# Kernel optimization log

Hardware: AMD Instinct MI355X
Metric: run time of the kernel (lower is better)

The kernel has to match this reference:

```python
import jax, jax.numpy as jnp
import numpy as np

NBITS = 3      # weight LSQ bits
PBITS = 8      # partial-sum LSQ bits
EPS = 1e-5


def round_ste(x):
    # straight-through round: identity gradient
    return x + jax.lax.stop_gradient(jnp.round(x) - x)


def lsq(x, alpha, nbits):
    # learned-step-size quantize/dequantize (symmetric signed)
    qn = -(2 ** (nbits - 1))
    qp = 2 ** (nbits - 1) - 1
    return round_ste(jnp.clip(x / alpha, qn, qp)) * alpha


def split_views(x):
    # x: [B,C,H,W] -> 9 shifted views of the 1-padded input, stacked [9,B,C,H,W]
    B, C, H, W = x.shape
    xp = jnp.pad(x, ((0, 0), (0, 0), (1, 1), (1, 1)))
    views = [xp[:, :, di:di + H, dj:dj + W] for dj in range(3) for di in range(3)]
    return jnp.stack(views, 0)


def split_conv3x3(x, w, wa, pa):
    # 3x3 conv emulated as 9 shifted 1x1 LSQ convs with quantized partial-sum accumulate
    # w: [9,O,C] per-tap 1x1 weights, wa: [9] weight step sizes, pa: [9] psum step sizes
    xs = split_views(x)                                      # [9,B,C,H,W]
    wq = jax.vmap(lambda wk, ak: lsq(wk, ak, NBITS))(w, wa)  # [9,O,C]
    ps = jnp.einsum('kbchw,koc->kbohw', xs, wq)              # 9 partial sums
    psq = lsq(ps, pa[:, None, None, None, None], PBITS)      # PartialSumLSQ each tap
    return psq.sum(0)                                        # accumulate -> [B,O,H,W]


def batchnorm(x, g, b):
    m = x.mean((0, 2, 3), keepdims=True)
    v = x.var((0, 2, 3), keepdims=True)
    return (x - m) / jnp.sqrt(v + EPS) * g[None, :, None, None] + b[None, :, None, None]


def setup_inputs() -> dict:
    key = jax.random.key(0)
    ks = jax.random.split(key, 8)
    B, C, O, H, W = 16, 128, 128, 56, 56
    x = jax.random.normal(ks[0], (B, C, H, W), jnp.float32)
    w1 = jax.random.normal(ks[1], (9, O, C), jnp.float32) * 0.05
    w2 = jax.random.normal(ks[2], (9, O, O), jnp.float32) * 0.05
    qp_w = 2 ** (NBITS - 1) - 1
    wa1 = 2.0 * jnp.mean(jnp.abs(w1), axis=(1, 2)) / np.sqrt(qp_w)
    wa2 = 2.0 * jnp.mean(jnp.abs(w2), axis=(1, 2)) / np.sqrt(qp_w)
    pa1 = jnp.full((9,), 0.05, jnp.float32)
    pa2 = jnp.full((9,), 0.05, jnp.float32)
    g1 = jnp.ones((O,), jnp.float32); b1 = jnp.zeros((O,), jnp.float32)
    g2 = jnp.ones((O,), jnp.float32); b2 = jnp.zeros((O,), jnp.float32)
    return {'x': x, 'w1': w1, 'wa1': wa1, 'pa1': pa1, 'g1': g1, 'b1': b1,
            'w2': w2, 'wa2': wa2, 'pa2': pa2, 'g2': g2, 'b2': b2}


def reference(x, w1, wa1, pa1, g1, b1, w2, wa2, pa2, g2, b2):
    identity = x
    out = split_conv3x3(x, w1, wa1, pa1)
    out = jax.nn.relu(batchnorm(out, g1, b1))
    out = split_conv3x3(out, w2, wa2, pa2)
    out = batchnorm(out, g2, b2)
    return jax.nn.relu(out + identity)
```

## Files before the change

### kernel.cpp

```cpp
#include <hip/hip_runtime.h>
#include <math.h>

typedef _Float16 f16;
typedef _Float16 half8 __attribute__((ext_vector_type(8)));
typedef float floatx16 __attribute__((ext_vector_type(16)));
typedef unsigned int u32;

#define HW_     3136
#define NPC     50176.0f
#define PB      3364
#define PPLANE  53824
#define ASTRIDE (2 * PPLANE * 16)

#define SW(c, px) (((px) + ((c) >> 2) + ((c) & 3) * 8) & 63)

typedef __attribute__((address_space(3))) u32 lds_u32;
typedef __attribute__((address_space(1))) u32 glb_u32;
__device__ __forceinline__ void async_copy16(const void* g, void* l) {
    __builtin_amdgcn_global_load_lds((const glb_u32*)g, (lds_u32*)l, 16, 0, 0);
}

__global__ __launch_bounds__(256) void setup_kernel(
        const float* __restrict__ w1, const float* __restrict__ wa1,
        const float* __restrict__ w2, const float* __restrict__ wa2,
        f16* __restrict__ W2a, f16* __restrict__ W2b, char* __restrict__ X2) {
    const int idx = blockIdx.x * 256 + threadIdx.x;
    if (idx < 36864) {
        const float* w;
        const float* wa;
        f16* o;
        int m;
        if (idx < 18432) { w = w1; wa = wa1; o = W2a; m = idx; }
        else             { w = w2; wa = wa2; o = W2b; m = idx - 18432; }
        const int tap = m >> 11;
        const int r = m & 2047;
        const int k2 = r >> 7;
        const int oc = r & 127;
        const float a = wa[tap];
        const float* src = w + ((size_t)(tap * 128 + oc) * 128 + k2 * 8);
        half8 hv;
#pragma unroll
        for (int j = 0; j < 8; ++j)
            hv[j] = (f16)rintf(fminf(fmaxf(src[j] / a, -4.f), 3.f));
        *(half8*)(o + (size_t)m * 8) = hv;
    } else {
        const int m = idx - 36864;
        const int k2 = m / 3648;
        const int r = m - k2 * 3648;
        const int b = r / 228;
        const int j = r - b * 228;
        int h, w;
        if (j < 58)        { h = 0;  w = j; }
        else if (j < 116)  { h = 57; w = j - 58; }
        else { const int k = j - 116; h = 1 + (k >> 1); w = (k & 1) * 57; }
        const size_t chunk = (size_t)k2 * PPLANE + (size_t)b * PB + h * 58 + w;
        float4 z = {0.f, 0.f, 0.f, 0.f};
        *(float4*)(X2 + chunk * 16) = z;
    }
}

__global__ __launch_bounds__(256) void pack_kernel(
        const float* __restrict__ x, char* __restrict__ X2,
        float* __restrict__ stats) {
    const int t = threadIdx.x;
    const int blk = blockIdx.x;
    if (blk == 0 && t < 512) stats[t] = 0.f;
    const int b = blk / 49;
    const int p0 = (blk - b * 49) * 64;
    const int px = t & 63;
    const int cq = t >> 6;
    const int p = p0 + px;
    const int h = p / 56;
    const int w = p - h * 56;
    const size_t pp = (size_t)b * PB + (h + 1) * 58 + (w + 1);
    const float* xb = x + (size_t)b * 128 * HW_ + p;
#pragma unroll
    for (int s = 0; s < 4; ++s) {
        const int cg = s * 4 + cq;
        half8 hv, lv;
#pragma unroll
        for (int j = 0; j < 8; ++j) {
            const float v = xb[(size_t)(cg * 8 + j) * HW_];
            const f16 hh = (f16)v;
            hv[j] = hh;
            lv[j] = (f16)(v - (float)hh);
        }
        *(half8*)(X2 + ((size_t)cg * PPLANE + pp) * 16) = hv;
        *(half8*)(X2 + ((size_t)(cg + 16) * PPLANE + pp) * 16) = lv;
    }
}

__global__ __launch_bounds__(256, 2) void conv_kernel(
        const char* __restrict__ X2, const char* __restrict__ W2,
        const float* __restrict__ wav, const float* __restrict__ pav,
        float* __restrict__ cbuf, float* __restrict__ stats) {
    __shared__ f16 Bls[2][16384];
    __shared__ float red[512];
    const int t = threadIdx.x;
    const int lane = t & 63;
    const int wv = t >> 6;
    const int wm = wv & 1, wn = wv >> 1;
    const int tile = (blockIdx.x & 7) * 98 + (blockIdx.x >> 3);
    const int kh = lane >> 5;
    const int ln = lane & 31;

    const int gp = tile * 64 + wm * 32 + ln;
    const int b = gp / HW_;
    const int p = gp - b * HW_;
    const int h = p / 56;
    const int w = p - h * 56;
    const int ppad = b * PB + (h + 1) * 58 + (w + 1);

    const int bdsoff0 = (kh * 128 + wn * 64 + ln) * 16;
    const int bdsoff1 = bdsoff0 + 32 * 16;
    const int sbase = wv * 8;

    floatx16 facc[2];
#pragma unroll
    for (int nt = 0; nt < 2; ++nt)
#pragma unroll
        for (int r = 0; r < 16; ++r) facc[nt][r] = 0.f;

#pragma unroll
    for (int i = 0; i < 8; ++i)
        async_copy16(W2 + (((sbase + i) * 64 + lane) << 4),
                     (void*)&Bls[0][(sbase + i) * 512]);
    const int aoff0 = ((ppad - 59) + kh * PPLANE) << 4;
    half8 afr[16];
#pragma unroll
    for (int c = 0; c < 16; ++c)
        afr[c] = *(const half8*)(X2 + aoff0 + c * ASTRIDE);
    __syncthreads();

    for (int tap = 0; tap < 9; ++tap) {
        const float pak = pav[tap];
        const float s1 = wav[tap] / pak;
        const char* bcur = (const char*)&Bls[tap & 1][0];
        int aoffn = 0;
        if (tap < 8) {
            const char* wt = W2 + (tap + 1) * 32768;
            f16* bnxt = &Bls[(tap + 1) & 1][0];
#pragma unroll
            for (int i = 0; i < 8; ++i)
                async_copy16(wt + (((sbase + i) * 64 + lane) << 4),
                             (void*)&bnxt[(sbase + i) * 512]);
            const int dn = ((tap + 1) % 3 - 1) * 58 + ((tap + 1) / 3 - 1);
            aoffn = ((ppad + dn) + kh * PPLANE) << 4;
        }
        half8 bds[2][8];
#pragma unroll
        for (int kf = 0; kf < 8; ++kf) {
            bds[0][kf] = *(const half8*)(bcur + kf * 4096 + bdsoff0);
            bds[1][kf] = *(const half8*)(bcur + kf * 4096 + bdsoff1);
        }

        floatx16 acc[2];
#pragma unroll
        for (int nt = 0; nt < 2; ++nt)
#pragma unroll
            for (int r = 0; r < 16; ++r) acc[nt][r] = 0.f;

#pragma unroll
        for (int s = 0; s < 16; ++s) {
            acc[0] = __builtin_amdgcn_mfma_f32_32x32x16_f16(
                afr[s], bds[0][s & 7], acc[0], 0, 0, 0);
            acc[1] = __builtin_amdgcn_mfma_f32_32x32x16_f16(
                afr[s], bds[1][s & 7], acc[1], 0, 0, 0);
            if (tap < 8)
                afr[s] = *(const half8*)(X2 + aoffn + s * ASTRIDE);
        }

#pragma unroll
        for (int nt = 0; nt < 2; ++nt)
#pragma unroll
            for (int r = 0; r < 16; ++r) {
                const float q = rintf(
                    __builtin_amdgcn_fmed3f(acc[nt][r] * s1, -128.f, 127.f));
                facc[nt][r] = fmaf(q, pak, facc[nt][r]);
            }
        __syncthreads();
    }

    const int gpb = tile * 64 + wm * 32;
#pragma unroll
    for (int r = 0; r < 16; ++r) {
        const int row = (r & 3) + 8 * (r >> 2) + 4 * kh;
        float* rp = cbuf + (size_t)(gpb + row) * 128 + wn * 64 + ln;
        rp[0]  = facc[0][r];
        rp[32] = facc[1][r];
    }

    float sv[2], qv[2];
#pragma unroll
    for (int nt = 0; nt < 2; ++nt) {
        float s = 0.f, q = 0.f;
#pragma unroll
        for (int r = 0; r < 16; ++r) {
            const float v = facc[nt][r];
            s += v;
            q = fmaf(v, v, q);
        }
        s += __shfl_xor(s, 32, 64);
        q += __shfl_xor(q, 32, 64);
        sv[nt] = s; qv[nt] = q;
    }
    if (lane < 32) {
#pragma unroll
        for (int nt = 0; nt < 2; ++nt) {
            const int oc = wn * 64 + nt * 32 + lane;
            red[oc * 2 + wm] = sv[nt];
            red[256 + oc * 2 + wm] = qv[nt];
        }
    }
    __syncthreads();
    if (t < 128) {
        atomicAdd(&stats[t],       red[2 * t] + red[2 * t + 1]);
        atomicAdd(&stats[128 + t], red[256 + 2 * t] + red[256 + 2 * t + 1]);
    }
}

__global__ __launch_bounds__(256) void bn_split_kernel(
        const float* __restrict__ cbuf, const float* __restrict__ stats,
        const float* __restrict__ g, const float* __restrict__ bb,
        char* __restrict__ X2) {
    __shared__ float xs[8192];
    __shared__ float scs[128], shs[128];
    const int t = threadIdx.x;
    if (t < 128) {
        const float m = stats[t] * (1.f / NPC);
        const float var = stats[128 + t] * (1.f / NPC) - m * m;
        const float inv = 1.f / sqrtf(var + 1e-5f);
        const float sc = g[t] * inv;
        scs[t] = sc;
        shs[t] = bb[t] - m * sc;
    }
    __syncthreads();
    const int blk = blockIdx.x;
#pragma unroll
    for (int i = 0; i < 8; ++i) {
        const int idx = i * 256 + t;
        const int px = idx >> 5;
        const int q = idx & 31;
        const float4 v = *(const float4*)&cbuf[(size_t)(blk * 64 + px) * 128 + q * 4];
        const float vv[4] = {v.x, v.y, v.z, v.w};
#pragma unroll
        for (int j = 0; j < 4; ++j) {
            const int c = q * 4 + j;
            xs[c * 64 + SW(c, px)] = fmaxf(fmaf(vv[j], scs[c], shs[c]), 0.f);
        }
    }
    __syncthreads();
    const int b = blk / 49;
    const int p0 = (blk - b * 49) * 64;
    const int px = t & 63;
    const int cq = t >> 6;
    const int p = p0 + px;
    const int h = p / 56;
    const int w = p - h * 56;
    const size_t pp = (size_t)b * PB + (h + 1) * 58 + (w + 1);
#pragma unroll
    for (int s = 0; s < 4; ++s) {
        const int cg = s * 4 + cq;
        half8 hv, lv;
#pragma unroll
        for (int j = 0; j < 8; ++j) {
            const int c = cg * 8 + j;
            const float v = xs[c * 64 + SW(c, px)];
            const f16 hh = (f16)v;
            hv[j] = hh;
            lv[j] = (f16)(v - (float)hh);
        }
        *(half8*)(X2 + ((size_t)cg * PPLANE + pp) * 16) = hv;
        *(half8*)(X2 + ((size_t)(cg + 16) * PPLANE + pp) * 16) = lv;
    }
}

__global__ __launch_bounds__(256) void final_kernel(
        const float* __restrict__ cbuf, const float* __restrict__ stats,
        const float* __restrict__ g, const float* __restrict__ bb,
        const float* __restrict__ resid, float* __restrict__ out) {
    __shared__ float xs[8192];
    __shared__ float scs[128], shs[128];
    const int t = threadIdx.x;
    if (t < 128) {
        const float m = stats[t] * (1.f / NPC);
        const float var = stats[128 + t] * (1.f / NPC) - m * m;
        const float inv = 1.f / sqrtf(var + 1e-5f);
        const float sc = g[t] * inv;
        scs[t] = sc;
        shs[t] = bb[t] - m * sc;
    }
    __syncthreads();
    const int blk = blockIdx.x;
#pragma unroll
    for (int i = 0; i < 8; ++i) {
        const int idx = i * 256 + t;
        const int px = idx >> 5;
        const int q = idx & 31;
        const float4 v = *(const float4*)&cbuf[(size_t)(blk * 64 + px) * 128 + q * 4];
        const float vv[4] = {v.x, v.y, v.z, v.w};
#pragma unroll
        for (int j = 0; j < 4; ++j) {
            const int c = q * 4 + j;
            xs[c * 64 + SW(c, px)] = fmaf(vv[j], scs[c], shs[c]);
        }
    }
    __syncthreads();
    const int b = blk / 49;
    const int p0 = (blk - b * 49) * 64;
    const int lane = t & 63, wq = t >> 6;
#pragma unroll
    for (int i = 0; i < 32; ++i) {
        const int c = i * 4 + wq;
        const float v = xs[c * 64 + SW(c, lane)];
        const size_t gi = (size_t)(b * 128 + c) * HW_ + p0 + lane;
        out[gi] = fmaxf(v + resid[gi], 0.f);
    }
}

extern "C" void kernel_launch(void* const* d_in, const int* in_sizes, int n_in,
                              void* d_out, int out_size, void* d_ws, size_t ws_size,
                              hipStream_t stream) {
    const float* x   = (const float*)d_in[0];
    const float* w1  = (const float*)d_in[1];
    const float* wa1 = (const float*)d_in[2];
    const float* pa1 = (const float*)d_in[3];
    const float* g1  = (const float*)d_in[4];
    const float* b1  = (const float*)d_in[5];
    const float* w2  = (const float*)d_in[6];
    const float* wa2 = (const float*)d_in[7];
    const float* pa2 = (const float*)d_in[8];
    const float* g2  = (const float*)d_in[9];
    const float* b2  = (const float*)d_in[10];
    float* out = (float*)d_out;

    char* ws = (char*)d_ws;
    char*  X2    = ws;
    float* cbuf  = (float*)(ws + 27557888);
    f16*   W2a   = (f16*)(ws + 53248000);
    f16*   W2b   = (f16*)(ws + 53542912);
    float* stats = (float*)(ws + 53837824);
    float* stats1 = stats;
    float* stats2 = stats + 256;

    hipLaunchKernelGGL(setup_kernel, dim3(600), dim3(256), 0, stream,
                       w1, wa1, w2, wa2, W2a, W2b, X2);
    hipLaunchKernelGGL(pack_kernel, dim3(784), dim3(256), 0, stream,
                       x, X2, stats);
    hipLaunchKernelGGL(conv_kernel, dim3(784), dim3(256), 0, stream,
                       X2, (const char*)W2a, wa1, pa1, cbuf, stats1);
    hipLaunchKernelGGL(bn_split_kernel, dim3(784), dim3(256), 0, stream,
                       cbuf, stats1, g1, b1, X2);
    hipLaunchKernelGGL(conv_kernel, dim3(784), dim3(256), 0, stream,
                       X2, (const char*)W2b, wa2, pa2, cbuf, stats2);
    hipLaunchKernelGGL(final_kernel, dim3(784), dim3(256), 0, stream,
                       cbuf, stats2, g2, b2, x, out);
}
```

Measured before the change: 230.7 us.

## Retile conv to 128px x 64oc blocks and merge setup with pack

Each conv block now covers 128 pixels with 4 waves stacked along M and only half of the output channels. That halves the per-tap weight tile in LDS and asks for 4 blocks per CU instead of 2. The stats reduction is rewritten to sum over 4 waves per channel half. Separately, the weight-quantize/border-zero setup kernel and the input pack kernel are merged into one launch to save a kernel boundary. The trade-off is that the activation fragments are now read by two blocks each, and the higher occupancy target may force register spills given the large per-thread fragment arrays.

```diff
diff --git a/kernel.cpp b/kernel.cpp
--- a/kernel.cpp
+++ b/kernel.cpp
@@ -20,12 +20,41 @@
     __builtin_amdgcn_global_load_lds((const glb_u32*)g, (lds_u32*)l, 16, 0, 0);
 }
 
-__global__ __launch_bounds__(256) void setup_kernel(
+__global__ __launch_bounds__(256) void prelude_kernel(
+        const float* __restrict__ x, char* __restrict__ X2,
         const float* __restrict__ w1, const float* __restrict__ wa1,
         const float* __restrict__ w2, const float* __restrict__ wa2,
-        f16* __restrict__ W2a, f16* __restrict__ W2b, char* __restrict__ X2) {
-    const int idx = blockIdx.x * 256 + threadIdx.x;
-    if (idx < 36864) {
+        f16* __restrict__ W2a, f16* __restrict__ W2b,
+        float* __restrict__ stats) {
+    const int t = threadIdx.x;
+    if (blockIdx.x < 784) {
+        const int blk = blockIdx.x;
+        if (blk == 0 && t < 512) stats[t] = 0.f;
+        const int b = blk / 49;
+        const int p0 = (blk - b * 49) * 64;
+        const int px = t & 63;
+        const int cq = t >> 6;
+        const int p = p0 + px;
+        const int h = p / 56;
+        const int w = p - h * 56;
+        const size_t pp = (size_t)b * PB + (h + 1) * 58 + (w + 1);
+        const float* xb = x + (size_t)b * 128 * HW_ + p;
+#pragma unroll
+        for (int s = 0; s < 4; ++s) {
+            const int cg = s * 4 + cq;
+            half8 hv, lv;
+#pragma unroll
+            for (int j = 0; j < 8; ++j) {
+                const float v = xb[(size_t)(cg * 8 + j) * HW_];
+                const f16 hh = (f16)v;
+                hv[j] = hh;
+                lv[j] = (f16)(v - (float)hh);
+            }
+            *(half8*)(X2 + ((size_t)cg * PPLANE + pp) * 16) = hv;
+            *(half8*)(X2 + ((size_t)(cg + 16) * PPLANE + pp) * 16) = lv;
+        }
+    } else if (blockIdx.x < 928) {
+        const int idx = (blockIdx.x - 784) * 256 + t;
         const float* w;
         const float* wa;
         f16* o;
@@ -44,7 +73,7 @@
             hv[j] = (f16)rintf(fminf(fmaxf(src[j] / a, -4.f), 3.f));
         *(half8*)(o + (size_t)m * 8) = hv;
     } else {
-        const int m = idx - 36864;
+        const int m = (blockIdx.x - 928) * 256 + t;
         const int k2 = m / 3648;
         const int r = m - k2 * 3648;
         const int b = r / 228;
@@ -59,61 +88,32 @@
     }
 }
 
-__global__ __launch_bounds__(256) void pack_kernel(
-        const float* __restrict__ x, char* __restrict__ X2,
-        float* __restrict__ stats) {
-    const int t = threadIdx.x;
-    const int blk = blockIdx.x;
-    if (blk == 0 && t < 512) stats[t] = 0.f;
-    const int b = blk / 49;
-    const int p0 = (blk - b * 49) * 64;
-    const int px = t & 63;
-    const int cq = t >> 6;
-    const int p = p0 + px;
-    const int h = p / 56;
-    const int w = p - h * 56;
-    const size_t pp = (size_t)b * PB + (h + 1) * 58 + (w + 1);
-    const float* xb = x + (size_t)b * 128 * HW_ + p;
-#pragma unroll
-    for (int s = 0; s < 4; ++s) {
-        const int cg = s * 4 + cq;
-        half8 hv, lv;
-#pragma unroll
-        for (int j = 0; j < 8; ++j) {
-            const float v = xb[(size_t)(cg * 8 + j) * HW_];
-            const f16 hh = (f16)v;
-            hv[j] = hh;
-            lv[j] = (f16)(v - (float)hh);
-        }
-        *(half8*)(X2 + ((size_t)cg * PPLANE + pp) * 16) = hv;
-        *(half8*)(X2 + ((size_t)(cg + 16) * PPLANE + pp) * 16) = lv;
-    }
-}
-
-__global__ __launch_bounds__(256, 2) void conv_kernel(
+__global__ __launch_bounds__(256, 4) void conv_kernel(
         const char* __restrict__ X2, const char* __restrict__ W2,
         const float* __restrict__ wav, const float* __restrict__ pav,
         float* __restrict__ cbuf, float* __restrict__ stats) {
-    __shared__ f16 Bls[2][16384];
+    __shared__ f16 Bls[2][8192];
     __shared__ float red[512];
     const int t = threadIdx.x;
     const int lane = t & 63;
     const int wv = t >> 6;
-    const int wm = wv & 1, wn = wv >> 1;
-    const int tile = (blockIdx.x & 7) * 98 + (blockIdx.x >> 3);
+    const int blk = (blockIdx.x & 7) * 98 + (blockIdx.x >> 3);
+    const int tile = blk >> 1;
+    const int oh = blk & 1;
     const int kh = lane >> 5;
     const int ln = lane & 31;
 
-    const int gp = tile * 64 + wm * 32 + ln;
+    const int gp = tile * 128 + wv * 32 + ln;
     const int b = gp / HW_;
     const int p = gp - b * HW_;
     const int h = p / 56;
     const int w = p - h * 56;
     const int ppad = b * PB + (h + 1) * 58 + (w + 1);
 
-    const int bdsoff0 = (kh * 128 + wn * 64 + ln) * 16;
+    const int bdsoff0 = kh * 1024 + ln * 16;
     const int bdsoff1 = bdsoff0 + 32 * 16;
-    const int sbase = wv * 8;
+    const int k2r0 = wv * 4;
+    const int socb = oh * 64;
 
     floatx16 facc[2];
 #pragma unroll
@@ -122,9 +122,9 @@
         for (int r = 0; r < 16; ++r) facc[nt][r] = 0.f;
 
 #pragma unroll
-    for (int i = 0; i < 8; ++i)
-        async_copy16(W2 + (((sbase + i) * 64 + lane) << 4),
-                     (void*)&Bls[0][(sbase + i) * 512]);
+    for (int i = 0; i < 4; ++i)
+        async_copy16(W2 + (((0 * 16 + k2r0 + i) * 128 + socb + lane) << 4),
+                     (void*)&Bls[0][(k2r0 + i) * 512]);
     const int aoff0 = ((ppad - 59) + kh * PPLANE) << 4;
     half8 afr[16];
 #pragma unroll
@@ -138,20 +138,20 @@
         const char* bcur = (const char*)&Bls[tap & 1][0];
         int aoffn = 0;
         if (tap < 8) {
-            const char* wt = W2 + (tap + 1) * 32768;
             f16* bnxt = &Bls[(tap + 1) & 1][0];
 #pragma unroll
-            for (int i = 0; i < 8; ++i)
-                async_copy16(wt + (((sbase + i) * 64 + lane) << 4),
-                             (void*)&bnxt[(sbase + i) * 512]);
+            for (int i = 0; i < 4; ++i)
+                async_copy16(
+                    W2 + ((((tap + 1) * 16 + k2r0 + i) * 128 + socb + lane) << 4),
+                    (void*)&bnxt[(k2r0 + i) * 512]);
             const int dn = ((tap + 1) % 3 - 1) * 58 + ((tap + 1) / 3 - 1);
             aoffn = ((ppad + dn) + kh * PPLANE) << 4;
         }
         half8 bds[2][8];
 #pragma unroll
         for (int kf = 0; kf < 8; ++kf) {
-            bds[0][kf] = *(const half8*)(bcur + kf * 4096 + bdsoff0);
-            bds[1][kf] = *(const half8*)(bcur + kf * 4096 + bdsoff1);
+            bds[0][kf] = *(const half8*)(bcur + kf * 2048 + bdsoff0);
+            bds[1][kf] = *(const half8*)(bcur + kf * 2048 + bdsoff1);
         }
 
         floatx16 acc[2];
@@ -181,11 +181,11 @@
         __syncthreads();
     }
 
-    const int gpb = tile * 64 + wm * 32;
+    const int gpb = tile * 128 + wv * 32;
 #pragma unroll
     for (int r = 0; r < 16; ++r) {
         const int row = (r & 3) + 8 * (r >> 2) + 4 * kh;
-        float* rp = cbuf + (size_t)(gpb + row) * 128 + wn * 64 + ln;
+        float* rp = cbuf + (size_t)(gpb + row) * 128 + oh * 64 + ln;
         rp[0]  = facc[0][r];
         rp[32] = facc[1][r];
     }
@@ -207,15 +207,17 @@
     if (lane < 32) {
 #pragma unroll
         for (int nt = 0; nt < 2; ++nt) {
-            const int oc = wn * 64 + nt * 32 + lane;
-            red[oc * 2 + wm] = sv[nt];
-            red[256 + oc * 2 + wm] = qv[nt];
-        }
-    }
-    __syncthreads();
-    if (t < 128) {
-        atomicAdd(&stats[t],       red[2 * t] + red[2 * t + 1]);
-        atomicAdd(&stats[128 + t], red[256 + 2 * t] + red[256 + 2 * t + 1]);
+            const int oc = nt * 32 + lane;
+            red[oc * 4 + wv] = sv[nt];
+            red[256 + oc * 4 + wv] = qv[nt];
+        }
+    }
+    __syncthreads();
+    if (t < 64) {
+        const float* r0 = &red[4 * t];
+        const float* r1 = &red[256 + 4 * t];
+        atomicAdd(&stats[oh * 64 + t],       r0[0] + r0[1] + r0[2] + r0[3]);
+        atomicAdd(&stats[128 + oh * 64 + t], r1[0] + r1[1] + r1[2] + r1[3]);
     }
 }
 
@@ -343,10 +345,8 @@
     float* stats1 = stats;
     float* stats2 = stats + 256;
 
-    hipLaunchKernelGGL(setup_kernel, dim3(600), dim3(256), 0, stream,
-                       w1, wa1, w2, wa2, W2a, W2b, X2);
-    hipLaunchKernelGGL(pack_kernel, dim3(784), dim3(256), 0, stream,
-                       x, X2, stats);
+    hipLaunchKernelGGL(prelude_kernel, dim3(1384), dim3(256), 0, stream,
+                       x, X2, w1, wa1, w2, wa2, W2a, W2b, stats);
     hipLaunchKernelGGL(conv_kernel, dim3(784), dim3(256), 0, stream,
                        X2, (const char*)W2a, wa1, pa1, cbuf, stats1);
     hipLaunchKernelGGL(bn_split_kernel, dim3(784), dim3(256), 0, stream,
```

Result: slower. 465.6 us (+101.8%).
